# Kernel tuning notes

Measured on AMD Instinct MI355X. Metric: run time of the kernel, lower is better.

## Reference

```python
import math
import jax, jax.numpy as jnp
import numpy as np

B, T = 4, 512
STATE_DIM, ACT_DIM = 17, 18
H, NH, L, MAXT = 1024, 16, 4, 4096
S = 3 * T          # interleaved (rtg, state, action) sequence length
D = H // NH
FF = 4 * H
LN_EPS = 1e-5


def setup_inputs() -> dict:
    key = jax.random.key(0)
    ks = jax.random.split(key, 32)
    init = lambda k, shape: jax.random.normal(k, shape, jnp.float32) * 0.02
    inp = {
        "states": jax.random.normal(ks[0], (B, T, STATE_DIM), jnp.float32),
        "returns_to_go": jax.random.normal(ks[1], (B, T, 1), jnp.float32),
        "timesteps": jax.random.randint(ks[2], (B, T), 0, MAXT),
        "actions": jax.random.randint(ks[3], (B, T), 0, ACT_DIM),
        "bandera": 0,
        # embeddings / input projections
        "embed_time_table": init(ks[4], (MAXT, H)),
        "embed_act_table": init(ks[5], (ACT_DIM, H)),
        "Wrtg": init(ks[6], (1, H)), "brtg": jnp.zeros((H,), jnp.float32),
        "Wst": init(ks[7], (STATE_DIM, H)), "bst": jnp.zeros((H,), jnp.float32),
        # per-block params, stacked over L layers
        "Wq": init(ks[8], (L, H, H)), "bq": jnp.zeros((L, H), jnp.float32),
        "Wk": init(ks[9], (L, H, H)), "bk": jnp.zeros((L, H), jnp.float32),
        "Wv": init(ks[10], (L, H, H)), "bv": jnp.zeros((L, H), jnp.float32),
        "Wo": init(ks[11], (L, H, H)), "bo": jnp.zeros((L, H), jnp.float32),
        "W1": init(ks[12], (L, H, FF)), "b1": jnp.zeros((L, FF), jnp.float32),
        "W2": init(ks[13], (L, FF, H)), "b2": jnp.zeros((L, H), jnp.float32),
        # prediction heads
        "Wpr": init(ks[14], (H, 1)), "bpr": jnp.zeros((1,), jnp.float32),
        "Wps": init(ks[15], (H, STATE_DIM)), "bps": jnp.zeros((STATE_DIM,), jnp.float32),
        "Wpa": init(ks[16], (H, ACT_DIM)), "bpa": jnp.zeros((ACT_DIM,), jnp.float32),
    }
    return inp


def _ln(x):
    # LayerNorm, elementwise_affine=False
    m = jnp.mean(x, axis=-1, keepdims=True)
    v = jnp.mean((x - m) ** 2, axis=-1, keepdims=True)
    return (x - m) * jax.lax.rsqrt(v + LN_EPS)


def reference(states, returns_to_go, embed_time_table, embed_act_table,
              Wrtg, brtg, Wst, bst,
              Wq, bq, Wk, bk, Wv, bv, Wo, bo,
              W1, b1, W2, b2,
              Wpr, bpr, Wps, bps, Wpa, bpa,
              timesteps, actions, bandera):
    te = embed_time_table[timesteps]                      # [B,T,H]
    r = returns_to_go @ Wrtg + brtg + te                  # [B,T,H]
    s = states @ Wst + bst + te                           # [B,T,H]
    a = embed_act_table[actions] + te                     # [B,T,H]
    # interleave (r_t, s_t, a_t) along time -> [B, 3T, H]
    h = jnp.stack([r, s, a], axis=2).reshape(B, S, H)
    h = _ln(h)
    mask = jnp.tril(jnp.ones((S, S), bool))
    scale = 1.0 / math.sqrt(D)
    for i in range(L):
        q = (h @ Wq[i] + bq[i]).reshape(B, S, NH, D).transpose(0, 2, 1, 3)
        k = (h @ Wk[i] + bk[i]).reshape(B, S, NH, D).transpose(0, 2, 1, 3)
        v = (h @ Wv[i] + bv[i]).reshape(B, S, NH, D).transpose(0, 2, 1, 3)
        sc = jnp.einsum('bhqd,bhkd->bhqk', q, k) * scale  # [B,NH,S,S]
        sc = jnp.where(mask, sc, -jnp.inf)
        att = jax.nn.softmax(sc, axis=-1)
        o = jnp.einsum('bhqk,bhkd->bhqd', att, v)
        o = o.transpose(0, 2, 1, 3).reshape(B, S, H)
        h = _ln(h + o @ Wo[i] + bo[i])
        m = jax.nn.gelu(h @ W1[i] + b1[i], approximate=False) @ W2[i] + b2[i]
        h = _ln(h + m)
    hh = h.reshape(B, T, 3, H)
    h_s = hh[:, :, 1]   # token after (..., r_t, s_t)
    h_a = hh[:, :, 2]   # token after (..., r_t, s_t, a_t)
    return_preds = h_a @ Wpr + bpr                        # [B,T,1]
    state_preds = h_a @ Wps + bps                         # [B,T,STATE_DIM]
    action_preds = h_s @ Wpa + bpa                        # [B,T,ACT_DIM]
    return (state_preds, action_preds, return_preds)
```

## Files before the change

### kernel.cpp

```cpp
#include <hip/hip_runtime.h>
#include <hip/hip_bf16.h>
#include <math.h>

#define Bc 4
#define Tc 512
#define Sc 1536
#define Hc 1024
#define NHc 16
#define Dc 64
#define FFc 4096
#define Lc 4
#define Mrows (Bc*Tc*3)
#define LN_EPS 1e-5f

typedef __attribute__((ext_vector_type(4))) float  f32x4;
typedef __attribute__((ext_vector_type(8))) short  s16x8;
typedef __attribute__((ext_vector_type(4))) short  s16x4;

__device__ __forceinline__ short f2b(float f) {
    union { __hip_bfloat16 h; short s; } u;
    u.h = __float2bfloat16(f);
    return u.s;
}

__device__ __forceinline__ void gload16(const void* g, void* l) {
    __builtin_amdgcn_global_load_lds(
        (const __attribute__((address_space(1))) void*)g,
        (__attribute__((address_space(3))) void*)l, 16, 0, 0);
}

__global__ __launch_bounds__(256) void embed_kernel(
    const float* __restrict__ states, const float* __restrict__ rtg,
    const int* __restrict__ timesteps, const int* __restrict__ actions,
    const float* __restrict__ ett, const float* __restrict__ eat,
    const float* __restrict__ Wrtg, const float* __restrict__ brtg,
    const float* __restrict__ Wst, const float* __restrict__ bst,
    float* __restrict__ h)
{
    const int bt = blockIdx.x;
    const int b = bt / Tc, t = bt % Tc;
    const int ts = timesteps[bt];
    const int ac = actions[bt];
    const float rv = rtg[bt];
    const float* te = ett + (size_t)ts * Hc;
    const float* ea = eat + (size_t)ac * Hc;
    __shared__ float sst[17];
    if (threadIdx.x < 17) sst[threadIdx.x] = states[bt * 17 + threadIdx.x];
    __syncthreads();
    float* hr = h + ((size_t)b * Sc + 3 * t) * Hc;
    for (int j = threadIdx.x; j < Hc; j += 256) {
        const float tej = te[j];
        hr[j] = rv * Wrtg[j] + brtg[j] + tej;
        float sv = bst[j];
        #pragma unroll
        for (int qx = 0; qx < 17; ++qx) sv += sst[qx] * Wst[qx * Hc + j];
        hr[Hc + j] = sv + tej;
        hr[2 * Hc + j] = ea[j] + tej;
    }
}

__global__ __launch_bounds__(256) void resln_kernel(float* __restrict__ h,
                                                    const float* __restrict__ add,
                                                    short* __restrict__ hb)
{
    const size_t row = blockIdx.x;
    float4* hr = reinterpret_cast<float4*>(h + row * Hc);
    const int tid = threadIdx.x;
    float4 x = hr[tid];
    if (add != nullptr) {
        const float4 a = reinterpret_cast<const float4*>(add + row * Hc)[tid];
        x.x += a.x; x.y += a.y; x.z += a.z; x.w += a.w;
    }
    float s1 = x.x + x.y + x.z + x.w;
    float s2 = x.x*x.x + x.y*x.y + x.z*x.z + x.w*x.w;
    #pragma unroll
    for (int off = 32; off > 0; off >>= 1) {
        s1 += __shfl_xor(s1, off);
        s2 += __shfl_xor(s2, off);
    }
    __shared__ float r1[4], r2[4];
    const int wv = tid >> 6, lane = tid & 63;
    if (lane == 0) { r1[wv] = s1; r2[wv] = s2; }
    __syncthreads();
    s1 = r1[0] + r1[1] + r1[2] + r1[3];
    s2 = r2[0] + r2[1] + r2[2] + r2[3];
    const float mean = s1 * (1.0f / Hc);
    const float var  = s2 * (1.0f / Hc) - mean * mean;
    const float rs = rsqrtf(var + LN_EPS);
    x.x = (x.x - mean) * rs; x.y = (x.y - mean) * rs;
    x.z = (x.z - mean) * rs; x.w = (x.w - mean) * rs;
    hr[tid] = x;
    if (hb != nullptr) {
        s16x4 o; o[0] = f2b(x.x); o[1] = f2b(x.y); o[2] = f2b(x.z); o[3] = f2b(x.w);
        *(s16x4*)&hb[row * Hc + tid * 4] = o;
    }
}

__global__ __launch_bounds__(256) void wconv_all_kernel(
    const float* __restrict__ Wq, const float* __restrict__ Wk,
    const float* __restrict__ Wv, const float* __restrict__ Wo,
    const float* __restrict__ W1, const float* __restrict__ W2,
    short* __restrict__ wqkv_t, short* __restrict__ wo_t,
    short* __restrict__ w1_t, short* __restrict__ w2_t)
{
    __shared__ float Ls[64][68];
    const int blk = blockIdx.x;
    const float* src; short* dst; int N, dstStride, dstRow0, tx, ty;
    if (blk < 1024) {
        const int m = blk >> 8;
        const int local = blk & 255;
        tx = local & 15; ty = local >> 4;
        N = 1024; dstStride = 1024;
        if (m == 0)      { src = Wq; dst = wqkv_t; dstRow0 = 0; }
        else if (m == 1) { src = Wk; dst = wqkv_t; dstRow0 = 1024; }
        else if (m == 2) { src = Wv; dst = wqkv_t; dstRow0 = 2048; }
        else             { src = Wo; dst = wo_t;   dstRow0 = 0; }
    } else if (blk < 2048) {
        const int local = blk - 1024;
        tx = local & 63; ty = local >> 6;
        src = W1; dst = w1_t; N = 4096; dstStride = 1024; dstRow0 = 0;
    } else {
        const int local = blk - 2048;
        tx = local & 15; ty = local >> 4;
        src = W2; dst = w2_t; N = 1024; dstStride = 4096; dstRow0 = 0;
    }
    const int n0 = tx * 64, k0 = ty * 64;
    const int tid = threadIdx.x;
    #pragma unroll
    for (int it = 0; it < 4; ++it) {
        const int idx = tid + 256 * it;
        const int r = idx >> 4, c4 = idx & 15;
        *(f32x4*)&Ls[r][c4 * 4] = *(const f32x4*)(src + (size_t)(k0 + r) * N + n0 + c4 * 4);
    }
    __syncthreads();
    #pragma unroll
    for (int it = 0; it < 2; ++it) {
        const int idx = tid + 256 * it;
        const int n = idx & 63, k8 = idx >> 6;
        s16x8 o;
        #pragma unroll
        for (int j = 0; j < 8; ++j) o[j] = f2b(Ls[k8 * 8 + j][n]);
        *(s16x8*)(dst + (size_t)(dstRow0 + n0 + n) * dstStride + k0 + k8 * 8) = o;
    }
}

__global__ __launch_bounds__(256) void biaspack_kernel(
    const float* __restrict__ bq, const float* __restrict__ bk,
    const float* __restrict__ bv, float* __restrict__ pb)
{
    const int idx = blockIdx.x * 256 + threadIdx.x;
    const int l = idx / 3072, j = idx % 3072;
    float v;
    if (j < 1024) v = bq[l * 1024 + j];
    else if (j < 2048) v = bk[l * 1024 + j - 1024];
    else v = bv[l * 1024 + j - 2048];
    pb[idx] = v;
}

__global__ __launch_bounds__(256) void headspack_kernel(
    const float* __restrict__ Wps, const float* __restrict__ bps,
    const float* __restrict__ Wpr, const float* __restrict__ bpr,
    const float* __restrict__ Wpa, const float* __restrict__ bpa,
    short* __restrict__ Wha, short* __restrict__ Whb,
    float* __restrict__ biasA, float* __restrict__ biasB)
{
    const int n = blockIdx.x & 63, set = blockIdx.x >> 6;
    const int tid = threadIdx.x;
    if (tid == 0) {
        if (set == 0) biasA[n] = (n < 17) ? bps[n] : (n == 17 ? bpr[0] : 0.f);
        else          biasB[n] = (n < 18) ? bpa[n] : 0.f;
    }
    short* dst = (set == 0 ? Wha : Whb) + (size_t)n * 1024;
    for (int k = tid; k < 1024; k += 256) {
        float v;
        if (set == 0) v = (n < 17) ? Wps[(size_t)k * 17 + n] : (n == 17 ? Wpr[k] : 0.f);
        else          v = (n < 18) ? Wpa[(size_t)k * 18 + n] : 0.f;
        dst[k] = f2b(v);
    }
}

__global__ __launch_bounds__(256) void headsgather_kernel(
    const float* __restrict__ scrA, const float* __restrict__ scrB,
    float* __restrict__ out)
{
    const int idx = blockIdx.x * 256 + threadIdx.x;
    if (idx >= 2048 * 36) return;
    const int bt = idx / 36, j = idx % 36;
    if (j < 17)      out[bt * 17 + j] = scrA[bt * 64 + j];
    else if (j < 35) out[2048 * 17 + bt * 18 + (j - 17)] = scrB[bt * 64 + (j - 17)];
    else             out[2048 * 35 + bt] = scrA[bt * 64 + 17];
}

template<int BN, int DO_GELU, int OUTBF16, int VT_FUSE>
__global__ __launch_bounds__(256, 4) void gemm_bb(
    const short* __restrict__ A, const short* __restrict__ Bt,
    const float* __restrict__ bias, void* __restrict__ Cv,
    int M, int N, int K, int arm, int aro, short* __restrict__ vt)
{
    constexpr int NJ = BN / 32;
    __shared__ short As[2 * 128 * 32];
    __shared__ short Bs[2 * BN * 32];
    const int tid = threadIdx.x, lane = tid & 63, wid = tid >> 6;
    const int wr = wid >> 1, wc = wid & 1;
    const int g = lane >> 4, ql = lane & 15;
    const int m0 = blockIdx.y * 128, n0 = blockIdx.x * BN;

    const int crow = lane >> 2;
    const int csw  = ((lane & 3) ^ ((crow >> 1) & 3)) * 8;

    const short* Ag0 = A + ((size_t)arm * (m0 + wid * 32 + crow) + aro) * K + csw;
    const short* Ag1 = A + ((size_t)arm * (m0 + wid * 32 + 16 + crow) + aro) * K + csw;
    const int a0off = (wid * 32) * 32;
    const int a1off = (wid * 32 + 16) * 32;

    const short* Bg0; const short* Bg1 = nullptr;
    int b0off = 0, b1off = 0;
    if constexpr (BN == 128) {
        Bg0 = Bt + (size_t)(n0 + wid * 32 + crow) * K + csw;
        Bg1 = Bt + (size_t)(n0 + wid * 32 + 16 + crow) * K + csw;
        b0off = (wid * 32) * 32;
        b1off = (wid * 32 + 16) * 32;
    } else {
        Bg0 = Bt + (size_t)(n0 + wid * 16 + crow) * K + csw;
        b0off = (wid * 16) * 32;
    }

    auto stage = [&](int buf, int k0) {
        short* Ab = &As[buf * (128 * 32)];
        short* Bb = &Bs[buf * (BN * 32)];
        gload16(Ag0 + k0, Ab + a0off);
        gload16(Ag1 + k0, Ab + a1off);
        gload16(Bg0 + k0, Bb + b0off);
        if constexpr (BN == 128) gload16(Bg1 + k0, Bb + b1off);
    };

    const int rslot = (g ^ ((ql >> 1) & 3)) * 8;
    const int aoffr = (wr * 64 + ql) * 32 + rslot;
    const int boffr = (wc * (BN / 2) + ql) * 32 + rslot;

    f32x4 acc[4][NJ] = {};
    stage(0, 0);
    stage(1, 32);
    int cur = 0;
    for (int k0 = 0; k0 < K; k0 += 32) {
        if (k0 + 32 < K) {
            if constexpr (BN == 128) asm volatile("s_waitcnt vmcnt(4)" ::: "memory");
            else                     asm volatile("s_waitcnt vmcnt(3)" ::: "memory");
        } else {
            asm volatile("s_waitcnt vmcnt(0)" ::: "memory");
        }
        __builtin_amdgcn_s_barrier();

        const short* Acur = &As[cur * (128 * 32)];
        const short* Bcur = &Bs[cur * (BN * 32)];
        s16x8 af[4], bfr[NJ];
        #pragma unroll
        for (int mi = 0; mi < 4; ++mi)
            af[mi] = *(const s16x8*)&Acur[aoffr + mi * (16 * 32)];
        #pragma unroll
        for (int nj = 0; nj < NJ; ++nj)
            bfr[nj] = *(const s16x8*)&Bcur[boffr + nj * (16 * 32)];

        asm volatile("s_waitcnt lgkmcnt(0)" ::: "memory");
        __builtin_amdgcn_sched_barrier(0);
        __builtin_amdgcn_s_barrier();

        if (k0 + 64 < K) stage(cur, k0 + 64);

        #pragma unroll
        for (int mi = 0; mi < 4; ++mi)
            #pragma unroll
            for (int nj = 0; nj < NJ; ++nj)
                acc[mi][nj] = __builtin_amdgcn_mfma_f32_16x16x32_bf16(
                    af[mi], bfr[nj], acc[mi][nj], 0, 0, 0);
        cur ^= 1;
    }

    #pragma unroll
    for (int mi = 0; mi < 4; ++mi) {
        #pragma unroll
        for (int nj = 0; nj < NJ; ++nj) {
            const int col = n0 + wc * (BN / 2) + nj * 16 + ql;
            const float bv = bias[col];
            float vals[4];
            #pragma unroll
            for (int r = 0; r < 4; ++r) {
                float v = acc[mi][nj][r] + bv;
                if constexpr (DO_GELU)
                    v = 0.5f * v * (1.0f + erff(v * 0.70710678118654752f));
                vals[r] = v;
            }
            if (VT_FUSE && col >= 2048) {
                const int row0 = m0 + wr * 64 + mi * 16 + g * 4;
                const int b = row0 / Sc, s = row0 % Sc;
                const int cc = col - 2048, hh = cc >> 6, d = cc & 63;
                s16x4 o;
                #pragma unroll
                for (int r = 0; r < 4; ++r) o[r] = f2b(vals[r]);
                *(s16x4*)(vt + (((size_t)(b * NHc + hh) * 64 + d) * Sc + s)) = o;
            } else {
                #pragma unroll
                for (int r = 0; r < 4; ++r) {
                    const int row = m0 + wr * 64 + mi * 16 + g * 4 + r;
                    if constexpr (OUTBF16)
                        ((short*)Cv)[(size_t)row * N + col] = f2b(vals[r]);
                    else
                        ((float*)Cv)[(size_t)row * N + col] = vals[r];
                }
            }
        }
    }
}

__global__ __launch_bounds__(256) void attn_kernel(
    const short* __restrict__ qg, const short* __restrict__ kg,
    const short* __restrict__ vtg, short* __restrict__ og, int qks)
{
    const int nqt = Sc / 64;
    const int blk = blockIdx.x;
    const int bh = blk / nqt;
    const int qt = (nqt - 1) - (blk % nqt);
    const int b = bh / NHc, hh = bh % NHc;
    const int tid = threadIdx.x, lane = tid & 63, w = tid >> 6;
    const int g = lane >> 4, ql = lane & 15;

    __shared__ short Ks[2][64 * 64];
    __shared__ short Vs[2][64 * 64];
    __shared__ short Qs[64][72];
    __shared__ short Ps[4][16][72];

    const size_t baseq = ((size_t)b * Sc) * qks + hh * Dc;

    #pragma unroll
    for (int i = 0; i < 2; ++i) {
        const int idx = tid + 256 * i;
        const int r = idx >> 3, c8 = idx & 7;
        *(s16x8*)&Qs[r][c8 * 8] =
            *(const s16x8*)(qg + baseq + (size_t)(qt * 64 + r) * qks + c8 * 8);
    }
    __syncthreads();
    const s16x8 bq0 = *(const s16x8*)&Qs[w * 16 + ql][g * 8];
    const s16x8 bq1 = *(const s16x8*)&Qs[w * 16 + ql][32 + g * 8];

    const int srow = lane >> 3;
    const int r0 = w * 8 + srow;
    const int r1 = 32 + w * 8 + srow;
    const int g0 = ((lane & 7) ^ (r0 & 7)) * 8;
    const int g1 = ((lane & 7) ^ (r1 & 7)) * 8;
    const short* kg0 = kg + baseq + (size_t)r0 * qks + g0;
    const short* kg1 = kg + baseq + (size_t)r1 * qks + g1;
    const short* vg0 = vtg + ((size_t)bh * 64 + r0) * Sc + g0;
    const short* vg1 = vtg + ((size_t)bh * 64 + r1) * Sc + g1;

    auto stageKV = [&](int buf, int kt) {
        const size_t ko = (size_t)kt * 64 * qks;
        const size_t vo = (size_t)kt * 64;
        gload16(kg0 + ko, &Ks[buf][w * 512]);
        gload16(kg1 + ko, &Ks[buf][2048 + w * 512]);
        gload16(vg0 + vo, &Vs[buf][w * 512]);
        gload16(vg1 + vo, &Vs[buf][2048 + w * 512]);
    };

    const int kx = ql & 7;
    const int gr0 = (g ^ kx) * 8;
    const int gr1 = ((4 + g) ^ kx) * 8;

    f32x4 acc_o[4] = {};
    float m = -1e30f, l = 0.f;
    const int qrow = qt * 64 + w * 16 + ql;

    stageKV(0, 0);
    for (int kt = 0; kt <= qt; ++kt) {
        const int buf = kt & 1;
        if (kt < qt) {
            stageKV(buf ^ 1, kt + 1);
            asm volatile("s_waitcnt vmcnt(4)" ::: "memory");
        } else {
            asm volatile("s_waitcnt vmcnt(0)" ::: "memory");
        }
        __builtin_amdgcn_s_barrier();

        s16x8 ka0[4], ka1[4], vv0[4], vv1[4];
        #pragma unroll
        for (int mi = 0; mi < 4; ++mi) {
            ka0[mi] = *(const s16x8*)&Ks[buf][(mi * 16 + ql) * 64 + gr0];
            ka1[mi] = *(const s16x8*)&Ks[buf][(mi * 16 + ql) * 64 + gr1];
            vv0[mi] = *(const s16x8*)&Vs[buf][(mi * 16 + ql) * 64 + gr0];
            vv1[mi] = *(const s16x8*)&Vs[buf][(mi * 16 + ql) * 64 + gr1];
        }
        asm volatile("s_waitcnt lgkmcnt(0)" ::: "memory");
        __builtin_amdgcn_sched_barrier(0);
        __builtin_amdgcn_s_barrier();

        f32x4 sacc[4] = {};
        #pragma unroll
        for (int mi = 0; mi < 4; ++mi) {
            sacc[mi] = __builtin_amdgcn_mfma_f32_16x16x32_bf16(ka0[mi], bq0, sacc[mi], 0, 0, 0);
            sacc[mi] = __builtin_amdgcn_mfma_f32_16x16x32_bf16(ka1[mi], bq1, sacc[mi], 0, 0, 0);
        }

        float pv[16];
        float pm = -1e30f;
        #pragma unroll
        for (int mi = 0; mi < 4; ++mi)
            #pragma unroll
            for (int r = 0; r < 4; ++r) {
                const int kv = kt * 64 + mi * 16 + g * 4 + r;
                const float s = (kv <= qrow) ? sacc[mi][r] * 0.125f : -1e30f;
                pv[mi * 4 + r] = s;
                pm = fmaxf(pm, s);
            }
        pm = fmaxf(pm, __shfl_xor(pm, 16));
        pm = fmaxf(pm, __shfl_xor(pm, 32));
        const float m2 = fmaxf(m, pm);
        const float corr = __expf(m - m2);
        m = m2;
        float ps = 0.f;
        #pragma unroll
        for (int i = 0; i < 16; ++i) { pv[i] = __expf(pv[i] - m2); ps += pv[i]; }
        ps += __shfl_xor(ps, 16);
        ps += __shfl_xor(ps, 32);
        l = l * corr + ps;

        #pragma unroll
        for (int mi = 0; mi < 4; ++mi) {
            s16x4 pw;
            #pragma unroll
            for (int r = 0; r < 4; ++r) pw[r] = f2b(pv[mi * 4 + r]);
            *(s16x4*)&Ps[w][ql][mi * 16 + g * 4] = pw;
        }

        float corr_r[4];
        #pragma unroll
        for (int r = 0; r < 4; ++r) corr_r[r] = __shfl(corr, g * 4 + r);
        #pragma unroll
        for (int nj = 0; nj < 4; ++nj)
            #pragma unroll
            for (int r = 0; r < 4; ++r) acc_o[nj][r] *= corr_r[r];

        const s16x8 pa0 = *(const s16x8*)&Ps[w][ql][g * 8];
        const s16x8 pa1 = *(const s16x8*)&Ps[w][ql][32 + g * 8];
        #pragma unroll
        for (int nj = 0; nj < 4; ++nj) {
            acc_o[nj] = __builtin_amdgcn_mfma_f32_16x16x32_bf16(pa0, vv0[nj], acc_o[nj], 0, 0, 0);
            acc_o[nj] = __builtin_amdgcn_mfma_f32_16x16x32_bf16(pa1, vv1[nj], acc_o[nj], 0, 0, 0);
        }
    }

    const float rl = 1.0f / l;
    float rl_r[4];
    #pragma unroll
    for (int r = 0; r < 4; ++r) rl_r[r] = __shfl(rl, g * 4 + r);
    const size_t baseo = ((size_t)b * Sc) * Hc + hh * Dc;
    #pragma unroll
    for (int nj = 0; nj < 4; ++nj)
        #pragma unroll
        for (int r = 0; r < 4; ++r) {
            const int qr = qt * 64 + w * 16 + g * 4 + r;
            og[baseo + (size_t)qr * Hc + nj * 16 + ql] = f2b(acc_o[nj][r] * rl_r[r]);
        }
}

extern "C" void kernel_launch(void* const* d_in, const int* in_sizes, int n_in,
                              void* d_out, int out_size, void* d_ws, size_t ws_size,
                              hipStream_t stream)
{
    const float* states = (const float*)d_in[0];
    const float* rtg    = (const float*)d_in[1];
    const int*   timesteps = (const int*)d_in[2];
    const int*   actions   = (const int*)d_in[3];
    const float* ett  = (const float*)d_in[5];
    const float* eat  = (const float*)d_in[6];
    const float* Wrtg = (const float*)d_in[7];
    const float* brtg = (const float*)d_in[8];
    const float* Wst  = (const float*)d_in[9];
    const float* bst  = (const float*)d_in[10];
    const float* Wq = (const float*)d_in[11];
    const float* bq = (const float*)d_in[12];
    const float* Wk = (const float*)d_in[13];
    const float* bk = (const float*)d_in[14];
    const float* Wv = (const float*)d_in[15];
    const float* bv = (const float*)d_in[16];
    const float* Wo = (const float*)d_in[17];
    const float* bo = (const float*)d_in[18];
    const float* W1 = (const float*)d_in[19];
    const float* b1 = (const float*)d_in[20];
    const float* W2 = (const float*)d_in[21];
    const float* b2 = (const float*)d_in[22];
    const float* Wpr = (const float*)d_in[23];
    const float* bpr = (const float*)d_in[24];
    const float* Wps = (const float*)d_in[25];
    const float* bps = (const float*)d_in[26];
    const float* Wpa = (const float*)d_in[27];
    const float* bpa = (const float*)d_in[28];
    float* out = (float*)d_out;

    char* wsb = (char*)d_ws;
    const size_t MH = (size_t)Mrows * Hc;
    const int nAttnBlk = Bc * NHc * (Sc / 64);

    const size_t off_h    = 0;
    const size_t off_hb   = off_h    + MH * 4;
    const size_t off_qkv  = off_hb   + MH * 2;
    const size_t off_vt   = off_qkv  + MH * 6;
    const size_t off_ob   = off_vt   + MH * 2;
    const size_t off_rb   = off_ob   + MH * 2;
    const size_t off_wl   = off_rb   + MH * 4;
    const size_t wl_qkv   = 0;
    const size_t wl_wo    = wl_qkv + (size_t)3072 * 1024 * 2;
    const size_t wl_w1    = wl_wo  + (size_t)1024 * 1024 * 2;
    const size_t wl_w2    = wl_w1  + (size_t)4096 * 1024 * 2;
    const size_t wl_bytes = wl_w2  + (size_t)1024 * 4096 * 2;
    const size_t off_pb   = off_wl + wl_bytes;

    float* h   = (float*)(wsb + off_h);
    short* hb  = (short*)(wsb + off_hb);
    short* qkv = (short*)(wsb + off_qkv);
    short* vt  = (short*)(wsb + off_vt);
    short* ob  = (short*)(wsb + off_ob);
    float* rb  = (float*)(wsb + off_rb);
    short* gb  = qkv;
    short* wqkv_t = (short*)(wsb + off_wl + wl_qkv);
    short* wo_t   = (short*)(wsb + off_wl + wl_wo);
    short* w1_t   = (short*)(wsb + off_wl + wl_w1);
    short* w2_t   = (short*)(wsb + off_wl + wl_w2);
    float* pb     = (float*)(wsb + off_pb);
    short* Wha   = ob;
    short* Whb   = ob + 64 * 1024;
    float* biasA = (float*)(ob + 2 * 64 * 1024);
    float* biasB = biasA + 64;
    float* scrA  = rb;
    float* scrB  = rb + 2048 * 64;

    biaspack_kernel<<<Lc * 12, 256, 0, stream>>>(bq, bk, bv, pb);
    embed_kernel<<<Bc * Tc, 256, 0, stream>>>(states, rtg, timesteps, actions,
                                              ett, eat, Wrtg, brtg, Wst, bst, h);
    resln_kernel<<<Mrows, 256, 0, stream>>>(h, nullptr, hb);

    const dim3 gQKV(3072 / 128, Mrows / 128);
    const dim3 gFF1(FFc / 128, Mrows / 128);
    const dim3 gN1K(1024 / 128, Mrows / 128);

    for (int i = 0; i < Lc; ++i) {
        const size_t wofH = (size_t)i * Hc * Hc;
        const size_t wofF = (size_t)i * Hc * FFc;
        wconv_all_kernel<<<3072, 256, 0, stream>>>(
            Wq + wofH, Wk + wofH, Wv + wofH, Wo + wofH, W1 + wofF, W2 + wofF,
            wqkv_t, wo_t, w1_t, w2_t);

        gemm_bb<128,0,1,1><<<gQKV, 256, 0, stream>>>(hb, wqkv_t, pb + i * 3072, qkv, Mrows, 3072, 1024, 1, 0, vt);
        attn_kernel<<<nAttnBlk, 256, 0, stream>>>(qkv, qkv + 1024, vt, ob, 3072);
        gemm_bb<128,0,0,0><<<gN1K, 256, 0, stream>>>(ob, wo_t, bo + i * Hc, rb, Mrows, 1024, 1024, 1, 0, nullptr);
        resln_kernel<<<Mrows, 256, 0, stream>>>(h, rb, hb);

        gemm_bb<128,1,1,0><<<gFF1, 256, 0, stream>>>(hb, w1_t, b1 + i * FFc, gb, Mrows, 4096, 1024, 1, 0, nullptr);
        gemm_bb<128,0,0,0><<<gN1K, 256, 0, stream>>>(gb, w2_t, b2 + i * Hc, rb, Mrows, 1024, 4096, 1, 0, nullptr);
        resln_kernel<<<Mrows, 256, 0, stream>>>(h, rb, hb);
    }

    headspack_kernel<<<128, 256, 0, stream>>>(Wps, bps, Wpr, bpr, Wpa, bpa,
                                              Wha, Whb, biasA, biasB);
    gemm_bb<64,0,0,0><<<dim3(1, 16), 256, 0, stream>>>(hb, Wha, biasA, scrA, 2048, 64, 1024, 3, 2, nullptr);
    gemm_bb<64,0,0,0><<<dim3(1, 16), 256, 0, stream>>>(hb, Whb, biasB, scrB, 2048, 64, 1024, 3, 1, nullptr);
    headsgather_kernel<<<288, 256, 0, stream>>>(scrA, scrB, out);
}
```

Before: 1.485 ms.

## Triple-buffer GEMM LDS pipeline and store residual GEMM outputs in bf16

The GEMM main loop moves from a double-buffered LDS scheme with two barriers per k-step to a three-buffer ring. The next-next tile is issued right after the single barrier, which removes one barrier per iteration and gives loads more time to land. The Wo and W2 GEMMs now write their outputs in bf16, and the residual LayerNorm kernel reads bf16, which halves the memory traffic for those intermediates. LDS use per block grows by half, which may reduce occupancy under the 4-blocks launch bound. Rounding the residual branch to bf16 also adds some numerical error.

```diff
diff --git a/kernel.cpp b/kernel.cpp
--- a/kernel.cpp
+++ b/kernel.cpp
@@ -21,6 +21,12 @@
     union { __hip_bfloat16 h; short s; } u;
     u.h = __float2bfloat16(f);
     return u.s;
+}
+
+__device__ __forceinline__ float b2f(short s) {
+    union { unsigned u; float f; } v;
+    v.u = ((unsigned)(unsigned short)s) << 16;
+    return v.f;
 }
 
 __device__ __forceinline__ void gload16(const void* g, void* l) {
@@ -60,7 +66,7 @@
 }
 
 __global__ __launch_bounds__(256) void resln_kernel(float* __restrict__ h,
-                                                    const float* __restrict__ add,
+                                                    const short* __restrict__ add,
                                                     short* __restrict__ hb)
 {
     const size_t row = blockIdx.x;
@@ -68,8 +74,8 @@
     const int tid = threadIdx.x;
     float4 x = hr[tid];
     if (add != nullptr) {
-        const float4 a = reinterpret_cast<const float4*>(add + row * Hc)[tid];
-        x.x += a.x; x.y += a.y; x.z += a.z; x.w += a.w;
+        const s16x4 a = *(const s16x4*)&add[row * Hc + tid * 4];
+        x.x += b2f(a[0]); x.y += b2f(a[1]); x.z += b2f(a[2]); x.w += b2f(a[3]);
     }
     float s1 = x.x + x.y + x.z + x.w;
     float s2 = x.x*x.x + x.y*x.y + x.z*x.z + x.w*x.w;
@@ -198,8 +204,8 @@
     int M, int N, int K, int arm, int aro, short* __restrict__ vt)
 {
     constexpr int NJ = BN / 32;
-    __shared__ short As[2 * 128 * 32];
-    __shared__ short Bs[2 * BN * 32];
+    __shared__ short As[3 * 128 * 32];
+    __shared__ short Bs[3 * BN * 32];
     const int tid = threadIdx.x, lane = tid & 63, wid = tid >> 6;
     const int wr = wid >> 1, wc = wid & 1;
     const int g = lane >> 4, ql = lane & 15;
@@ -239,11 +245,12 @@
     const int boffr = (wc * (BN / 2) + ql) * 32 + rslot;
 
     f32x4 acc[4][NJ] = {};
+    const int NT = K / 32;
     stage(0, 0);
     stage(1, 32);
-    int cur = 0;
-    for (int k0 = 0; k0 < K; k0 += 32) {
-        if (k0 + 32 < K) {
+    int buf = 0;
+    for (int t = 0; t < NT; ++t) {
+        if (t + 1 < NT) {
             if constexpr (BN == 128) asm volatile("s_waitcnt vmcnt(4)" ::: "memory");
             else                     asm volatile("s_waitcnt vmcnt(3)" ::: "memory");
         } else {
@@ -251,8 +258,13 @@
         }
         __builtin_amdgcn_s_barrier();
 
-        const short* Acur = &As[cur * (128 * 32)];
-        const short* Bcur = &Bs[cur * (BN * 32)];
+        if (t + 2 < NT) {
+            const int nb = (buf + 2 >= 3) ? buf - 1 : buf + 2;
+            stage(nb, (t + 2) * 32);
+        }
+
+        const short* Acur = &As[buf * (128 * 32)];
+        const short* Bcur = &Bs[buf * (BN * 32)];
         s16x8 af[4], bfr[NJ];
         #pragma unroll
         for (int mi = 0; mi < 4; ++mi)
@@ -263,9 +275,6 @@
 
         asm volatile("s_waitcnt lgkmcnt(0)" ::: "memory");
         __builtin_amdgcn_sched_barrier(0);
-        __builtin_amdgcn_s_barrier();
-
-        if (k0 + 64 < K) stage(cur, k0 + 64);
 
         #pragma unroll
         for (int mi = 0; mi < 4; ++mi)
@@ -273,7 +282,7 @@
             for (int nj = 0; nj < NJ; ++nj)
                 acc[mi][nj] = __builtin_amdgcn_mfma_f32_16x16x32_bf16(
                     af[mi], bfr[nj], acc[mi][nj], 0, 0, 0);
-        cur ^= 1;
+        buf = (buf + 1 == 3) ? 0 : buf + 1;
     }
 
     #pragma unroll
@@ -518,7 +527,7 @@
     short* qkv = (short*)(wsb + off_qkv);
     short* vt  = (short*)(wsb + off_vt);
     short* ob  = (short*)(wsb + off_ob);
-    float* rb  = (float*)(wsb + off_rb);
+    short* rb  = (short*)(wsb + off_rb);
     short* gb  = qkv;
     short* wqkv_t = (short*)(wsb + off_wl + wl_qkv);
     short* wo_t   = (short*)(wsb + off_wl + wl_wo);
@@ -529,8 +538,8 @@
     short* Whb   = ob + 64 * 1024;
     float* biasA = (float*)(ob + 2 * 64 * 1024);
     float* biasB = biasA + 64;
-    float* scrA  = rb;
-    float* scrB  = rb + 2048 * 64;
+    float* scrA  = (float*)(wsb + off_rb + MH * 2);
+    float* scrB  = scrA + 2048 * 64;
 
     biaspack_kernel<<<Lc * 12, 256, 0, stream>>>(bq, bk, bv, pb);
     embed_kernel<<<Bc * Tc, 256, 0, stream>>>(states, rtg, timesteps, actions,
@@ -550,11 +559,11 @@
 
         gemm_bb<128,0,1,1><<<gQKV, 256, 0, stream>>>(hb, wqkv_t, pb + i * 3072, qkv, Mrows, 3072, 1024, 1, 0, vt);
         attn_kernel<<<nAttnBlk, 256, 0, stream>>>(qkv, qkv + 1024, vt, ob, 3072);
-        gemm_bb<128,0,0,0><<<gN1K, 256, 0, stream>>>(ob, wo_t, bo + i * Hc, rb, Mrows, 1024, 1024, 1, 0, nullptr);
+        gemm_bb<128,0,1,0><<<gN1K, 256, 0, stream>>>(ob, wo_t, bo + i * Hc, rb, Mrows, 1024, 1024, 1, 0, nullptr);
         resln_kernel<<<Mrows, 256, 0, stream>>>(h, rb, hb);
 
         gemm_bb<128,1,1,0><<<gFF1, 256, 0, stream>>>(hb, w1_t, b1 + i * FFc, gb, Mrows, 4096, 1024, 1, 0, nullptr);
-        gemm_bb<128,0,0,0><<<gN1K, 256, 0, stream>>>(gb, w2_t, b2 + i * Hc, rb, Mrows, 1024, 4096, 1, 0, nullptr);
+        gemm_bb<128,0,1,0><<<gN1K, 256, 0, stream>>>(gb, w2_t, b2 + i * Hc, rb, Mrows, 1024, 4096, 1, 0, nullptr);
         resln_kernel<<<Mrows, 256, 0, stream>>>(h, rb, hb);
     }
 
```

Result: slower. 1.554 ms (+4.7%).
